# Optimization experiments

Hardware: AMD Instinct MI355X
Metric: run time of the kernel (lower is better)

The kernel has to match this reference:

```python
import jax, jax.numpy as jnp
import numpy as np

NBINS = 30  # matches init kwarg `bins`


def setup_inputs() -> dict:
    key = jax.random.key(0)
    k1, k2, k3, k4 = jax.random.split(key, 4)
    B, C, Q, D = 128, 4, 32, 2048
    # cosine-similarity matrix in [-1, 1): required so bin indices land in [0, NBINS)
    simmat = jax.random.uniform(k1, (B, C, Q, D), jnp.float32, minval=-1.0, maxval=1.0)
    dlens = jax.random.randint(k2, (B,), 1, D, dtype=jnp.int32)
    # token ids; -1 marks padding (masked out of the histogram weights)
    dtoks = jax.random.randint(k3, (B, D), -1, 100, dtype=jnp.int32)
    qtoks = jax.random.randint(k4, (B, Q), -1, 100, dtype=jnp.int32)
    return {"simmat": simmat, "dlens": dlens, "dtoks": dtoks, "qtoks": qtoks}


def reference(simmat, dlens, dtoks, qtoks):
    B, C, Q, D = simmat.shape
    # bin index per similarity value; torch's .int() truncates toward zero,
    # which equals astype(int32) here since all values are non-negative.
    bins = ((simmat + 1.00001) / 2.0 * (NBINS - 1)).astype(jnp.int32)  # [B,C,Q,D]
    # padding mask: count a (q,d) pair only if both tokens are valid
    w = ((dtoks != -1)[:, None, :] & (qtoks != -1)[:, :, None]).astype(jnp.float32)  # [B,Q,D]
    w4 = jnp.broadcast_to(w[:, None, :, :], (B, C, Q, D))
    # weighted bincount per (b,c,q) row via one flat scatter-add
    rows = jnp.arange(B * C * Q, dtype=jnp.int32)[:, None]            # [BCQ,1]
    flat_idx = (rows * NBINS + bins.reshape(B * C * Q, D)).reshape(-1)
    hist = jnp.zeros((B * C * Q * NBINS,), jnp.float32).at[flat_idx].add(w4.reshape(-1))
    return hist.reshape(B, C, Q, NBINS)
```

## Files before the change

kernel.cpp:

```cpp
#include <hip/hip_runtime.h>


#define NBINS  30
#define DIM    2048
#define QDIM   32
#define CDIM   4
#define BDIM   128
#define GSTRIDE 33
#define WSTRIDE (8 * GSTRIDE)

typedef float nfloat4 __attribute__((ext_vector_type(4)));
typedef int   nint4   __attribute__((ext_vector_type(4)));

__global__ __launch_bounds__(256) void CountHistogram_kernel(
    const float* __restrict__ simmat,
    const int*   __restrict__ dtoks,
    const int*   __restrict__ qtoks,
    float*       __restrict__ out)
{
    const int tid  = threadIdx.x;
    const int wave = tid >> 6;
    const int lane = tid & 63;
    const int row  = blockIdx.x * 4 + wave;
    const int q    = row & (QDIM - 1);
    const int b    = row >> 7;

    __shared__ int hs[4 * WSTRIDE];
    int* hw = hs + wave * WSTRIDE;
    hw[lane] = 0; hw[lane + 64] = 0; hw[lane + 128] = 0; hw[lane + 192] = 0;
    if (lane < WSTRIDE - 256) hw[lane + 256] = 0;

    const int qt = qtoks[b * QDIM + q];
    int* hg = hw + (lane >> 3) * GSTRIDE;

    if (qt != -1) {
        const nfloat4* sm = (const nfloat4*)(simmat + (size_t)row * DIM);
        const nint4*   dt = (const nint4*)(dtoks  + (size_t)b   * DIM);
        #pragma unroll
        for (int j = 0; j < 8; ++j) {
            const nfloat4 s = __builtin_nontemporal_load(&sm[j * 64 + lane]);
            const nint4   t = dt[j * 64 + lane];
            int b0 = (int)((s.x + 1.00001f) / 2.0f * 29.0f);
            int b1 = (int)((s.y + 1.00001f) / 2.0f * 29.0f);
            int b2 = (int)((s.z + 1.00001f) / 2.0f * 29.0f);
            int b3 = (int)((s.w + 1.00001f) / 2.0f * 29.0f);
            b0 = (t.x != -1) ? b0 : 31;
            b1 = (t.y != -1) ? b1 : 31;
            b2 = (t.z != -1) ? b2 : 31;
            b3 = (t.w != -1) ? b3 : 31;
            atomicAdd(&hg[b0], 1);
            atomicAdd(&hg[b1], 1);
            atomicAdd(&hg[b2], 1);
            atomicAdd(&hg[b3], 1);
        }
    }

    if (lane < NBINS) {
        int sum = 0;
        #pragma unroll
        for (int g = 0; g < 8; ++g)
            sum += hw[g * GSTRIDE + lane];
        out[(size_t)row * NBINS + lane] = (float)sum;
    }
}

extern "C" void kernel_launch(void* const* d_in, const int* in_sizes, int n_in,
                              void* d_out, int out_size, void* d_ws, size_t ws_size,
                              hipStream_t stream) {
    const float* simmat = (const float*)d_in[0];
    const int*   dtoks  = (const int*)d_in[2];
    const int*   qtoks  = (const int*)d_in[3];
    float*       out    = (float*)d_out;

    const int nrows = BDIM * CDIM * QDIM;
    CountHistogram_kernel<<<nrows / 4, 256, 0, stream>>>(simmat, dtoks, qtoks, out);
}
```

Baseline: 27.54 us.

## Process two rows per wave and reuse a packed dtoks validity bitmask

Each wave now builds histograms for two (b,c,q) rows instead of one. The dtoks validity for the shared batch row is loaded once and packed into a 32-bit bitmask that both rows reuse, so the per-row dtoks loads go away. The bin computation folds the divide-by-two and multiply into a single multiply by 14.5, which could change rounding at bin boundaries in rare cases. It launches half as many blocks, uses twice the shared memory per block, and adds a launch-bounds occupancy hint. The kernel was already bound by the simmat stream, so the saving may be small.

```diff
diff --git a/kernel.cpp b/kernel.cpp
--- a/kernel.cpp
+++ b/kernel.cpp
@@ -1,53 +1,69 @@
 #include <hip/hip_runtime.h>
 
 
-#define NBINS  30
-#define DIM    2048
-#define QDIM   32
-#define CDIM   4
-#define BDIM   128
+#define NBINS   30
+#define DIM     2048
+#define QDIM    32
+#define CDIM    4
+#define BDIM    128
 #define GSTRIDE 33
 #define WSTRIDE (8 * GSTRIDE)
+#define ROWS    2
 
 typedef float nfloat4 __attribute__((ext_vector_type(4)));
 typedef int   nint4   __attribute__((ext_vector_type(4)));
 
-__global__ __launch_bounds__(256) void CountHistogram_kernel(
+__global__ __launch_bounds__(256, 4) void CountHistogram_kernel(
     const float* __restrict__ simmat,
     const int*   __restrict__ dtoks,
     const int*   __restrict__ qtoks,
     float*       __restrict__ out)
 {
-    const int tid  = threadIdx.x;
-    const int wave = tid >> 6;
-    const int lane = tid & 63;
-    const int row  = blockIdx.x * 4 + wave;
-    const int q    = row & (QDIM - 1);
-    const int b    = row >> 7;
+    const int tid   = threadIdx.x;
+    const int wave  = tid >> 6;
+    const int lane  = tid & 63;
+    const int rbase = (blockIdx.x * 4 + wave) * ROWS;
+    const int b     = rbase >> 7;
 
-    __shared__ int hs[4 * WSTRIDE];
-    int* hw = hs + wave * WSTRIDE;
-    hw[lane] = 0; hw[lane + 64] = 0; hw[lane + 128] = 0; hw[lane + 192] = 0;
-    if (lane < WSTRIDE - 256) hw[lane + 256] = 0;
+    __shared__ int hs[4][ROWS][WSTRIDE];
+    int* hw = &hs[wave][0][0];
+    #pragma unroll
+    for (int z = 0; z < 8; ++z) hw[z * 64 + lane] = 0;
+    if (lane < 2 * WSTRIDE - 512) hw[512 + lane] = 0;
 
-    const int qt = qtoks[b * QDIM + q];
-    int* hg = hw + (lane >> 3) * GSTRIDE;
+    const nint4* dt = (const nint4*)(dtoks + (size_t)b * DIM);
+    unsigned int mask = 0;
+    #pragma unroll
+    for (int j = 0; j < 8; ++j) {
+        const nint4 t = dt[j * 64 + lane];
+        unsigned int nib = (unsigned int)(t.x != -1)
+                         | ((unsigned int)(t.y != -1) << 1)
+                         | ((unsigned int)(t.z != -1) << 2)
+                         | ((unsigned int)(t.w != -1) << 3);
+        mask |= nib << (4 * j);
+    }
 
-    if (qt != -1) {
+    const int grpoff = (lane >> 3) * GSTRIDE;
+
+    #pragma unroll
+    for (int r = 0; r < ROWS; ++r) {
+        const int row = rbase + r;
+        const int qt  = qtoks[b * QDIM + (row & (QDIM - 1))];
+        const unsigned int rm = (qt != -1) ? mask : 0u;
+        int* hg = &hs[wave][r][0] + grpoff;
         const nfloat4* sm = (const nfloat4*)(simmat + (size_t)row * DIM);
-        const nint4*   dt = (const nint4*)(dtoks  + (size_t)b   * DIM);
         #pragma unroll
         for (int j = 0; j < 8; ++j) {
             const nfloat4 s = __builtin_nontemporal_load(&sm[j * 64 + lane]);
-            const nint4   t = dt[j * 64 + lane];
-            int b0 = (int)((s.x + 1.00001f) / 2.0f * 29.0f);
-            int b1 = (int)((s.y + 1.00001f) / 2.0f * 29.0f);
-            int b2 = (int)((s.z + 1.00001f) / 2.0f * 29.0f);
-            int b3 = (int)((s.w + 1.00001f) / 2.0f * 29.0f);
-            b0 = (t.x != -1) ? b0 : 31;
-            b1 = (t.y != -1) ? b1 : 31;
-            b2 = (t.z != -1) ? b2 : 31;
-            b3 = (t.w != -1) ? b3 : 31;
+            const unsigned int nib = rm >> (4 * j);
+            int b0 = (int)((s.x + 1.00001f) * 14.5f);
+            int b1 = (int)((s.y + 1.00001f) * 14.5f);
+            int b2 = (int)((s.z + 1.00001f) * 14.5f);
+            int b3 = (int)((s.w + 1.00001f) * 14.5f);
+            b0 = (nib & 1u) ? b0 : 31;
+            b1 = (nib & 2u) ? b1 : 31;
+            b2 = (nib & 4u) ? b2 : 31;
+            b3 = (nib & 8u) ? b3 : 31;
             atomicAdd(&hg[b0], 1);
             atomicAdd(&hg[b1], 1);
             atomicAdd(&hg[b2], 1);
@@ -56,11 +72,14 @@
     }
 
     if (lane < NBINS) {
-        int sum = 0;
         #pragma unroll
-        for (int g = 0; g < 8; ++g)
-            sum += hw[g * GSTRIDE + lane];
-        out[(size_t)row * NBINS + lane] = (float)sum;
+        for (int r = 0; r < ROWS; ++r) {
+            int sum = 0;
+            #pragma unroll
+            for (int g = 0; g < 8; ++g)
+                sum += hs[wave][r][g * GSTRIDE + lane];
+            out[(size_t)(rbase + r) * NBINS + lane] = (float)sum;
+        }
     }
 }
 
@@ -73,5 +92,5 @@
     float*       out    = (float*)d_out;
 
     const int nrows = BDIM * CDIM * QDIM;
-    CountHistogram_kernel<<<nrows / 4, 256, 0, stream>>>(simmat, dtoks, qtoks, out);
+    CountHistogram_kernel<<<nrows / (4 * ROWS), 256, 0, stream>>>(simmat, dtoks, qtoks, out);
 }
```

After: 29.68 us. +7.8%, slower.
